# Kernel optimization log

Measured on AMD Instinct MI355X. Metric: run time of the kernel, lower is better.

Reference implementation:

```python
import jax, jax.numpy as jnp
import numpy as np

THRESHOLD = 0.3          # config.sparse_threshold
COMPETITION_FACTOR = 2.0 # config.competition_factor
TARGET_SPARSITY = 0.1    # config.target_sparsity


def setup_inputs() -> dict:
    key = jax.random.key(0)
    B, D = 32768, 1024
    H = D // 4
    ks = jax.random.split(key, 18)
    def lin(k, fan_in, shape):
        return jax.random.normal(k, shape, dtype=jnp.float32) / np.sqrt(fan_in)
    return {
        "features": jax.random.normal(ks[0], (B, D), dtype=jnp.float32),
        # sparse_gating: Linear(D, D//4) -> ReLU -> Linear(D//4, D) -> Sigmoid
        "w_g1": lin(ks[1], D, (D, H)), "b_g1": jnp.zeros((H,), jnp.float32),
        "w_g2": lin(ks[2], H, (H, D)), "b_g2": jnp.zeros((D,), jnp.float32),
        # competition_calculator: Linear(D, D) -> ReLU -> Linear(D, 1) -> Sigmoid
        "w_c1": lin(ks[3], D, (D, D)), "b_c1": jnp.zeros((D,), jnp.float32),
        "w_c2": lin(ks[4], D, (D, 1)), "b_c2": jnp.zeros((1,), jnp.float32),
        # sparsity_feedback: Linear(2, 16) -> ReLU -> Linear(16, D) -> Sigmoid
        "w_r1": lin(ks[5], 2, (2, 16)), "b_r1": jnp.zeros((16,), jnp.float32),
        "w_r2": lin(ks[6], 16, (16, D)), "b_r2": jnp.zeros((D,), jnp.float32),
        # adaptive_threshold: Linear(3, 16) -> ReLU -> Linear(16, 1) -> Sigmoid
        "w_m1": lin(ks[7], 3, (3, 16)), "b_m1": jnp.zeros((16,), jnp.float32),
        "w_m2": lin(ks[8], 16, (16, 1)), "b_m2": jnp.zeros((1,), jnp.float32),
    }


def _competitive_sparse(f, w_c1, b_c1, w_c2, b_c2):
    # competition_strength: [B, 1] scalar per row (output Linear has out_dim 1)
    c = jax.nn.sigmoid(jax.nn.relu(f @ w_c1 + b_c1) @ w_c2 + b_c2)  # [B,1]
    inh = COMPETITION_FACTOR * c                                     # [B,1]
    # other_activations_j = f_j * (1 - inh) for j != i, and f_i at position i.
    scaled = f * (1.0 - inh)                                         # [B,D]
    # max over j != i of scaled_j, vectorized via top-2
    top2_vals, _ = jax.lax.top_k(scaled, 2)                          # [B,2]
    am = jnp.argmax(scaled, axis=-1)                                 # [B]
    idx = jnp.arange(f.shape[-1])
    max_excl = jnp.where(idx[None, :] == am[:, None],
                         top2_vals[:, 1:2], top2_vals[:, 0:1])       # [B,D]
    other_max = jnp.maximum(f, max_excl)                             # includes own f_i term
    win = other_max < f
    return jnp.where(f > THRESHOLD, jnp.where(win, f, 0.0), f)


def reference(features, w_g1, b_g1, w_g2, b_g2, w_c1, b_c1, w_c2, b_c2,
              w_r1, b_r1, w_r2, b_r2, w_m1, b_m1, w_m2, b_m2):
    # 1) sparse gating
    gw = jax.nn.sigmoid(jax.nn.relu(features @ w_g1 + b_g1) @ w_g2 + b_g2)
    gated = features * gw
    # 2) competitive sparse activation
    comp = _competitive_sparse(gated, w_c1, b_c1, w_c2, b_c2)
    # 3) dynamic sparsity regulation
    cur_sp = jnp.mean((jnp.abs(comp) < 0.1).astype(comp.dtype), axis=-1)  # [B]
    sp_in = jnp.stack([cur_sp, jnp.full_like(cur_sp, TARGET_SPARSITY)], axis=-1)  # [B,2]
    rw = jax.nn.sigmoid(jax.nn.relu(sp_in @ w_r1 + b_r1) @ w_r2 + b_r2)  # [B,D]
    dyn = comp * rw
    # 4) adaptive threshold (monitor); torch.std is unbiased -> ddof=1
    fmean = jnp.mean(dyn, axis=-1, keepdims=True)
    fstd = jnp.std(dyn, axis=-1, ddof=1, keepdims=True)
    fmax = jnp.max(dyn, axis=-1, keepdims=True)
    thr_in = jnp.concatenate([fmean, fstd, fmax], axis=-1)            # [B,3]
    thr = jax.nn.sigmoid(jax.nn.relu(thr_in @ w_m1 + b_m1) @ w_m2 + b_m2)  # [B,1]
    # 5) final sparse mask
    mask = (jnp.abs(dyn) > thr).astype(dyn.dtype)
    return dyn * mask
```

## Files before the change

### kernel.cpp

```cpp
#include <hip/hip_runtime.h>
#include <cmath>

#define TM 128
#define TN 128
#define TK 16
#define LDSW 132
#define FIXCAP 262144u
#define ROWCAP 32768u

#define B03  2.5e-5f
#define B01  2.5e-5f
#define B2   5e-6
#define BDYN 3e-5f

#define STAGE_STORE(B)                                                          \
        As[B][aq * 4 + 0][ar] = pa0.x; As[B][aq * 4 + 1][ar] = pa0.y;           \
        As[B][aq * 4 + 2][ar] = pa0.z; As[B][aq * 4 + 3][ar] = pa0.w;           \
        As[B][aq * 4 + 0][ar + 64] = pa1.x; As[B][aq * 4 + 1][ar + 64] = pa1.y; \
        As[B][aq * 4 + 2][ar + 64] = pa1.z; As[B][aq * 4 + 3][ar + 64] = pa1.w; \
        *(float4*)&Bs[B][bk][bn4] = pb0;                                        \
        *(float4*)&Bs[B][bk + 8][bn4] = pb1;

#define GEMM_MAINLOOP(Aptr, Wptr, Kdim, Ndim)                                   \
    __shared__ float As[2][TK][LDSW];                                           \
    __shared__ float Bs[2][TK][LDSW];                                           \
    const int tid = threadIdx.x;                                                \
    const int bm = blockIdx.x * TM;                                             \
    const int bn = blockIdx.y * TN;                                             \
    const int tx = tid & 15, ty = tid >> 4;                                     \
    const int ar = tid >> 2, aq = tid & 3;                                      \
    const int bk = tid >> 5, bn4 = (tid & 31) * 4;                              \
    float acc[2][2][4][4];                                                      \
    _Pragma("unroll") for (int a = 0; a < 2; ++a)                               \
    _Pragma("unroll") for (int b = 0; b < 2; ++b)                               \
    _Pragma("unroll") for (int i = 0; i < 4; ++i)                               \
    _Pragma("unroll") for (int j = 0; j < 4; ++j) acc[a][b][i][j] = 0.f;        \
    float4 pa0 = *(const float4*)((Aptr) + (size_t)(bm + ar) * (Kdim) + aq * 4);      \
    float4 pa1 = *(const float4*)((Aptr) + (size_t)(bm + ar + 64) * (Kdim) + aq * 4); \
    float4 pb0 = *(const float4*)((Wptr) + (size_t)bk * (Ndim) + bn + bn4);           \
    float4 pb1 = *(const float4*)((Wptr) + (size_t)(bk + 8) * (Ndim) + bn + bn4);     \
    STAGE_STORE(0)                                                              \
    __syncthreads();                                                            \
    int buf = 0;                                                                \
    for (int k0 = 0; k0 < (Kdim); k0 += TK) {                                   \
        const int nk = k0 + TK;                                                 \
        if (nk < (Kdim)) {                                                      \
            pa0 = *(const float4*)((Aptr) + (size_t)(bm + ar) * (Kdim) + nk + aq * 4);      \
            pa1 = *(const float4*)((Aptr) + (size_t)(bm + ar + 64) * (Kdim) + nk + aq * 4); \
            pb0 = *(const float4*)((Wptr) + (size_t)(nk + bk) * (Ndim) + bn + bn4);         \
            pb1 = *(const float4*)((Wptr) + (size_t)(nk + bk + 8) * (Ndim) + bn + bn4);     \
        }                                                                       \
        _Pragma("unroll") for (int k = 0; k < TK; ++k) {                        \
            float4 da0 = *(const float4*)&As[buf][k][ty * 4];                   \
            float4 da1 = *(const float4*)&As[buf][k][64 + ty * 4];              \
            float4 db0 = *(const float4*)&Bs[buf][k][tx * 4];                   \
            float4 db1 = *(const float4*)&Bs[buf][k][64 + tx * 4];              \
            const float* dap[2] = {&da0.x, &da1.x};                             \
            const float* dbp[2] = {&db0.x, &db1.x};                             \
            _Pragma("unroll") for (int a = 0; a < 2; ++a)                       \
            _Pragma("unroll") for (int b = 0; b < 2; ++b)                       \
            _Pragma("unroll") for (int i = 0; i < 4; ++i)                       \
            _Pragma("unroll") for (int j = 0; j < 4; ++j)                       \
                acc[a][b][i][j] = fmaf(dap[a][i], dbp[b][j], acc[a][b][i][j]);  \
        }                                                                       \
        if (nk < (Kdim)) {                                                      \
            const int nb = buf ^ 1;                                             \
            STAGE_STORE(nb)                                                     \
            __syncthreads();                                                    \
            buf = nb;                                                           \
        }                                                                       \
    }

__global__ __launch_bounds__(256) void gemm1_f32(
    const float* __restrict__ A, const float* __restrict__ W,
    const float* __restrict__ bias, float* __restrict__ out, int M)
{
    const int K = 1024, N = 256;
    GEMM_MAINLOOP(A, W, K, N)
    #pragma unroll
    for (int a = 0; a < 2; ++a) {
        #pragma unroll
        for (int b = 0; b < 2; ++b) {
            const int col = bn + b * 64 + tx * 4;
            float4 bi = *(const float4*)(bias + col);
            #pragma unroll
            for (int i = 0; i < 4; ++i) {
                const int row = bm + a * 64 + ty * 4 + i;
                float4 o;
                o.x = fmaxf(acc[a][b][i][0] + bi.x, 0.f);
                o.y = fmaxf(acc[a][b][i][1] + bi.y, 0.f);
                o.z = fmaxf(acc[a][b][i][2] + bi.z, 0.f);
                o.w = fmaxf(acc[a][b][i][3] + bi.w, 0.f);
                *(float4*)(out + (size_t)row * N + col) = o;
            }
        }
    }
}

__global__ __launch_bounds__(256) void gemm2_f32(
    const float* __restrict__ A, const float* __restrict__ W,
    const float* __restrict__ bias, const float* __restrict__ F,
    float* __restrict__ out, unsigned* __restrict__ ectr1,
    uint2* __restrict__ elist1, int M)
{
    const int K = 256, N = 1024;
    GEMM_MAINLOOP(A, W, K, N)
    #pragma unroll
    for (int a = 0; a < 2; ++a) {
        #pragma unroll
        for (int b = 0; b < 2; ++b) {
            const int col = bn + b * 64 + tx * 4;
            float4 bi = *(const float4*)(bias + col);
            const float* bip = &bi.x;
            #pragma unroll
            for (int i = 0; i < 4; ++i) {
                const int row = bm + a * 64 + ty * 4 + i;
                float4 fv = *(const float4*)(F + (size_t)row * N + col);
                const float* fvp = &fv.x;
                float4 o;
                float* op = &o.x;
                #pragma unroll
                for (int j = 0; j < 4; ++j) {
                    float z = acc[a][b][i][j] + bip[j];
                    float gw = 1.0f / (1.0f + __expf(-z));
                    float g = fvp[j] * gw;
                    float c = (g > 0.3f) ? 0.f : g;
                    if (fabsf(g - 0.3f) < B03 || fabsf(fabsf(c) - 0.1f) < B01) {
                        unsigned idx = atomicAdd(ectr1, 1u);
                        if (idx < FIXCAP) elist1[idx] = make_uint2((unsigned)row, (unsigned)(col + j));
                    }
                    op[j] = c;
                }
                *(float4*)(out + (size_t)row * N + col) = o;
            }
        }
    }
}

__global__ __launch_bounds__(256) void fix_near(
    const float* __restrict__ h1, const float* __restrict__ F,
    const float* __restrict__ Wg2, const float* __restrict__ bg2,
    const unsigned* __restrict__ ectr1, const uint2* __restrict__ elist1,
    unsigned* __restrict__ ectr2, uint2* __restrict__ elist2,
    float* __restrict__ out, int* __restrict__ corr)
{
    __shared__ double red[4];
    const int tid = threadIdx.x;
    unsigned cnt = *ectr1;
    if (cnt > FIXCAP) cnt = FIXCAP;

    for (unsigned e = blockIdx.x; e < cnt; e += gridDim.x) {
        const unsigned row = elist1[e].x, col = elist1[e].y;
        double p = (double)h1[(size_t)row * 256 + tid]
                 * (double)Wg2[(size_t)tid * 1024 + col];
        #pragma unroll
        for (int o = 32; o > 0; o >>= 1) p += __shfl_down(p, o, 64);
        if ((tid & 63) == 0) red[tid >> 6] = p;
        __syncthreads();
        if (tid == 0) {
            double z2 = red[0] + red[1] + red[2] + red[3] + (double)bg2[col];
            double gw = 1.0 / (1.0 + exp(-z2));
            double g = (double)F[(size_t)row * 1024 + col] * gw;
            double c = (g > 0.3) ? 0.0 : g;
            bool near = (fabs(g - 0.3) < B2) || (fabs(fabs(c) - 0.1) < B2);
            if (near) {
                unsigned i2 = atomicAdd(ectr2, 1u);
                if (i2 < FIXCAP) elist2[i2] = make_uint2(row, col);
            } else {
                float cf = (float)c;
                int d_ref = (fabs(c) < 0.1) ? 1 : 0;
                int d_st  = (fabsf(cf) < 0.1f) ? 1 : 0;
                if (d_ref != d_st) atomicAdd(&corr[row], d_ref - d_st);
                out[(size_t)row * 1024 + col] = cf;
            }
        }
        __syncthreads();
    }
}

#define WT_PREFETCH(ptr)                                                        \
            r0 = *(const float4*)((ptr) + 0 * 1024 + tid * 4);                  \
            r1 = *(const float4*)((ptr) + 1 * 1024 + tid * 4);                  \
            r2 = *(const float4*)((ptr) + 2 * 1024 + tid * 4);                  \
            r3 = *(const float4*)((ptr) + 3 * 1024 + tid * 4);

#define WT_STORE(B)                                                             \
            *(float4*)&Wt[B][0 * 1024 + tid * 4] = r0;                          \
            *(float4*)&Wt[B][1 * 1024 + tid * 4] = r1;                          \
            *(float4*)&Wt[B][2 * 1024 + tid * 4] = r2;                          \
            *(float4*)&Wt[B][3 * 1024 + tid * 4] = r3;

__global__ __launch_bounds__(256) void fix_full(
    const float* __restrict__ F, const float* __restrict__ Wg1,
    const float* __restrict__ bg1, const float* __restrict__ Wg2,
    const float* __restrict__ bg2,
    const unsigned* __restrict__ ectr2, const uint2* __restrict__ elist2,
    float* __restrict__ out, int* __restrict__ corr)
{
    __shared__ float Fs[1024];
    __shared__ float Wt[2][4096];
    __shared__ double red[4];
    const int tid = threadIdx.x;
    unsigned cnt = *ectr2;
    if (cnt > FIXCAP) cnt = FIXCAP;

    for (unsigned e = blockIdx.x; e < cnt; e += gridDim.x) {
        const unsigned row = elist2[e].x, col = elist2[e].y;
        __syncthreads();
        *(float4*)&Fs[tid * 4] = *(const float4*)(F + (size_t)row * 1024 + tid * 4);

        float4 r0, r1, r2, r3;
        WT_PREFETCH(Wg1)
        WT_STORE(0)
        __syncthreads();
        double p0 = 0.0, p1 = 0.0, p2 = 0.0, p3 = 0.0;
        int buf = 0;
        for (int t = 0; t < 64; ++t) {
            if (t + 1 < 64) { const float* np = Wg1 + (size_t)(t + 1) * 4096; WT_PREFETCH(np) }
            const int kb = t * 16;
            #pragma unroll
            for (int kk = 0; kk < 16; kk += 4) {
                p0 += (double)Fs[kb + kk + 0] * (double)Wt[buf][(kk + 0) * 256 + tid];
                p1 += (double)Fs[kb + kk + 1] * (double)Wt[buf][(kk + 1) * 256 + tid];
                p2 += (double)Fs[kb + kk + 2] * (double)Wt[buf][(kk + 2) * 256 + tid];
                p3 += (double)Fs[kb + kk + 3] * (double)Wt[buf][(kk + 3) * 256 + tid];
            }
            if (t + 1 < 64) {
                const int nb = buf ^ 1;
                WT_STORE(nb)
                __syncthreads();
                buf = nb;
            }
        }
        double h = ((p0 + p1) + (p2 + p3)) + (double)bg1[tid];
        h = (h > 0.0) ? h : 0.0;
        double p = h * (double)Wg2[(size_t)tid * 1024 + col];
        #pragma unroll
        for (int o = 32; o > 0; o >>= 1) p += __shfl_down(p, o, 64);
        if ((tid & 63) == 0) red[tid >> 6] = p;
        __syncthreads();
        if (tid == 0) {
            double z2 = red[0] + red[1] + red[2] + red[3] + (double)bg2[col];
            double gw = 1.0 / (1.0 + exp(-z2));
            double g = (double)Fs[col] * gw;
            double c = (g > 0.3) ? 0.0 : g;
            float cf = (float)c;
            int d_ref = (fabs(c) < 0.1) ? 1 : 0;
            int d_st  = (fabsf(cf) < 0.1f) ? 1 : 0;
            if (d_ref != d_st) atomicAdd(&corr[row], d_ref - d_st);
            out[(size_t)row * 1024 + col] = cf;
        }
    }
}

__global__ __launch_bounds__(256) void finalize_rows(
    float* __restrict__ C,
    const float* __restrict__ wr1, const float* __restrict__ br1,
    const float* __restrict__ wr2, const float* __restrict__ br2,
    const float* __restrict__ wm1, const float* __restrict__ bm1,
    const float* __restrict__ wm2, const float* __restrict__ bm2,
    const int* __restrict__ corr,
    unsigned* __restrict__ rctr, unsigned* __restrict__ rowlist)
{
    const int D = 1024;
    const int tid = threadIdx.x;
    const int lane = tid & 63;
    const unsigned row = blockIdx.x * 4 + (tid >> 6);
    const size_t base = (size_t)row * D;
    const int col0 = lane * 4;

    float4 c4[4];
    #pragma unroll
    for (int q = 0; q < 4; ++q)
        c4[q] = *(const float4*)(C + base + q * 256 + col0);

    float c[16];
    #pragma unroll
    for (int q = 0; q < 4; ++q) {
        c[q * 4 + 0] = c4[q].x; c[q * 4 + 1] = c4[q].y;
        c[q * 4 + 2] = c4[q].z; c[q * 4 + 3] = c4[q].w;
    }

    float cnt = 0.f;
    #pragma unroll
    for (int i = 0; i < 16; ++i) cnt += (fabsf(c[i]) < 0.1f) ? 1.f : 0.f;
    #pragma unroll
    for (int o = 32; o > 0; o >>= 1) cnt += __shfl_xor(cnt, o, 64);
    cnt += (float)corr[row];
    const double cur_sp = (double)cnt / 1024.0;

    float hid[16];
    #pragma unroll
    for (int h = 0; h < 16; ++h) {
        double z = cur_sp * (double)wr1[h] + 0.1 * (double)wr1[16 + h] + (double)br1[h];
        hid[h] = (float)((z > 0.0) ? z : 0.0);
    }

    float dyn[16];
    #pragma unroll
    for (int q = 0; q < 4; ++q) {
        const int cq = q * 256 + col0;
        float4 b4 = *(const float4*)(br2 + cq);
        float z[4] = {b4.x, b4.y, b4.z, b4.w};
        #pragma unroll
        for (int h = 0; h < 16; ++h) {
            float4 w4 = *(const float4*)(wr2 + (size_t)h * D + cq);
            z[0] = fmaf(hid[h], w4.x, z[0]);
            z[1] = fmaf(hid[h], w4.y, z[1]);
            z[2] = fmaf(hid[h], w4.z, z[2]);
            z[3] = fmaf(hid[h], w4.w, z[3]);
        }
        #pragma unroll
        for (int j = 0; j < 4; ++j) {
            float rw = 1.0f / (1.0f + __expf(-z[j]));
            dyn[q * 4 + j] = c[q * 4 + j] * rw;
        }
    }

    float s = 0.f, mx = -1e30f;
    #pragma unroll
    for (int i = 0; i < 16; ++i) { s += dyn[i]; mx = fmaxf(mx, dyn[i]); }
    #pragma unroll
    for (int o = 32; o > 0; o >>= 1) s += __shfl_xor(s, o, 64);
    const float mean = s / 1024.0f;

    float sq = 0.f;
    #pragma unroll
    for (int i = 0; i < 16; ++i) { float d = dyn[i] - mean; sq = fmaf(d, d, sq); }
    #pragma unroll
    for (int o = 32; o > 0; o >>= 1) sq += __shfl_xor(sq, o, 64);
    const float sd = sqrtf(sq / 1023.0f);

    #pragma unroll
    for (int o = 32; o > 0; o >>= 1) mx = fmaxf(mx, __shfl_xor(mx, o, 64));

    double acc2 = (double)bm2[0];
    #pragma unroll
    for (int h = 0; h < 16; ++h) {
        double hz = (double)mean * (double)wm1[h] + (double)sd * (double)wm1[16 + h]
                  + (double)mx * (double)wm1[32 + h] + (double)bm1[h];
        hz = (hz > 0.0) ? hz : 0.0;
        acc2 += hz * (double)wm2[h];
    }
    const float thr = (float)(1.0 / (1.0 + exp(-acc2)));

    bool fl = false;
    #pragma unroll
    for (int i = 0; i < 16; ++i)
        if (fabsf(fabsf(dyn[i]) - thr) < BDYN) fl = true;

    if (__any(fl)) {
        if (lane == 0) {
            unsigned idx = atomicAdd(rctr, 1u);
            if (idx < ROWCAP) rowlist[idx] = row;
        }
        return;
    }

    #pragma unroll
    for (int q = 0; q < 4; ++q) {
        float4 o4;
        float* op = &o4.x;
        #pragma unroll
        for (int j = 0; j < 4; ++j) {
            float d = dyn[q * 4 + j];
            op[j] = (fabsf(d) > thr) ? d : 0.f;
        }
        *(float4*)(C + base + q * 256 + col0) = o4;
    }
}

__device__ __forceinline__ double block_reduce_d(double v, double* sm, int tid, int op)
{
    #pragma unroll
    for (int o = 32; o > 0; o >>= 1) {
        double other = __shfl_down(v, o, 64);
        v = op ? fmax(v, other) : (v + other);
    }
    if ((tid & 63) == 0) sm[tid >> 6] = v;
    __syncthreads();
    if (tid == 0) {
        double r = sm[0];
        for (int w = 1; w < 4; ++w) r = op ? fmax(r, sm[w]) : (r + sm[w]);
        sm[4] = r;
    }
    __syncthreads();
    double r = sm[4];
    __syncthreads();
    return r;
}

__global__ __launch_bounds__(256) void row_exact(
    const float* __restrict__ F,
    const float* __restrict__ wg1, const float* __restrict__ bg1,
    const float* __restrict__ wg2, const float* __restrict__ bg2,
    const float* __restrict__ wr1, const float* __restrict__ br1,
    const float* __restrict__ wr2, const float* __restrict__ br2,
    const float* __restrict__ wm1, const float* __restrict__ bm1,
    const float* __restrict__ wm2, const float* __restrict__ bm2,
    const unsigned* __restrict__ rctr, const unsigned* __restrict__ rowlist,
    float* __restrict__ out)
{
    __shared__ float  Fs[1024];
    __shared__ float  Wt[2][4096];
    __shared__ double h1d[256];
    __shared__ double sm[8];
    const int tid = threadIdx.x;
    unsigned rcnt = *rctr;
    if (rcnt > ROWCAP) rcnt = ROWCAP;

    for (unsigned e = blockIdx.x; e < rcnt; e += gridDim.x) {
        const unsigned row = rowlist[e];
        __syncthreads();
        *(float4*)&Fs[tid * 4] = *(const float4*)(F + (size_t)row * 1024 + tid * 4);

        {
            float4 r0, r1, r2, r3;
            WT_PREFETCH(wg1)
            WT_STORE(0)
            __syncthreads();
            double p0 = 0.0, p1 = 0.0, p2 = 0.0, p3 = 0.0;
            int buf = 0;
            for (int t = 0; t < 64; ++t) {
                if (t + 1 < 64) { const float* np = wg1 + (size_t)(t + 1) * 4096; WT_PREFETCH(np) }
                const int kb = t * 16;
                #pragma unroll
                for (int kk = 0; kk < 16; kk += 4) {
                    p0 += (double)Fs[kb + kk + 0] * (double)Wt[buf][(kk + 0) * 256 + tid];
                    p1 += (double)Fs[kb + kk + 1] * (double)Wt[buf][(kk + 1) * 256 + tid];
                    p2 += (double)Fs[kb + kk + 2] * (double)Wt[buf][(kk + 2) * 256 + tid];
                    p3 += (double)Fs[kb + kk + 3] * (double)Wt[buf][(kk + 3) * 256 + tid];
                }
                if (t + 1 < 64) {
                    const int nb = buf ^ 1;
                    WT_STORE(nb)
                    __syncthreads();
                    buf = nb;
                }
            }
            double a = ((p0 + p1) + (p2 + p3)) + (double)bg1[tid];
            h1d[tid] = (a > 0.0) ? a : 0.0;
        }
        __syncthreads();

        const int c0 = tid * 4;
        double zA[4] = {0.0, 0.0, 0.0, 0.0};
        double zB[4] = {0.0, 0.0, 0.0, 0.0};
        {
            float4 r0, r1, r2, r3;
            WT_PREFETCH(wg2)
            WT_STORE(0)
            __syncthreads();
            int buf = 0;
            for (int t = 0; t < 64; ++t) {
                if (t + 1 < 64) { const float* np = wg2 + (size_t)(t + 1) * 4096; WT_PREFETCH(np) }
                const int jb = t * 4;
                #pragma unroll
                for (int kk = 0; kk < 4; kk += 2) {
                    float4 wA = *(const float4*)&Wt[buf][(kk + 0) * 1024 + c0];
                    float4 wB = *(const float4*)&Wt[buf][(kk + 1) * 1024 + c0];
                    double hA = h1d[jb + kk], hB = h1d[jb + kk + 1];
                    zA[0] += hA * (double)wA.x; zA[1] += hA * (double)wA.y;
                    zA[2] += hA * (double)wA.z; zA[3] += hA * (double)wA.w;
                    zB[0] += hB * (double)wB.x; zB[1] += hB * (double)wB.y;
                    zB[2] += hB * (double)wB.z; zB[3] += hB * (double)wB.w;
                }
                if (t + 1 < 64) {
                    const int nb = buf ^ 1;
                    WT_STORE(nb)
                    __syncthreads();
                    buf = nb;
                }
            }
        }
        double comp[4];
        double cnt = 0.0;
        #pragma unroll
        for (int j = 0; j < 4; ++j) {
            double z2v = (double)bg2[c0 + j] + zA[j] + zB[j];
            double gw = 1.0 / (1.0 + exp(-z2v));
            double g = (double)Fs[c0 + j] * gw;
            double cm = (g > 0.3) ? 0.0 : g;
            comp[j] = cm;
            cnt += (fabs(cm) < 0.1) ? 1.0 : 0.0;
        }
        cnt = block_reduce_d(cnt, sm, tid, 0);
        const double cur_sp = cnt / 1024.0;

        double hid[16];
        #pragma unroll
        for (int h = 0; h < 16; ++h) {
            double hz = cur_sp * (double)wr1[h] + 0.1 * (double)wr1[16 + h] + (double)br1[h];
            hid[h] = (hz > 0.0) ? hz : 0.0;
        }
        double zr[4] = {(double)br2[c0], (double)br2[c0 + 1],
                        (double)br2[c0 + 2], (double)br2[c0 + 3]};
        #pragma unroll
        for (int h = 0; h < 16; ++h) {
            float4 w4 = *(const float4*)(wr2 + (size_t)h * 1024 + c0);
            zr[0] += hid[h] * (double)w4.x; zr[1] += hid[h] * (double)w4.y;
            zr[2] += hid[h] * (double)w4.z; zr[3] += hid[h] * (double)w4.w;
        }
        double dyn[4];
        #pragma unroll
        for (int j = 0; j < 4; ++j) {
            double rw = 1.0 / (1.0 + exp(-zr[j]));
            dyn[j] = comp[j] * rw;
        }

        double s = dyn[0] + dyn[1] + dyn[2] + dyn[3];
        s = block_reduce_d(s, sm, tid, 0);
        const double mean = s / 1024.0;

        double sq = 0.0;
        #pragma unroll
        for (int j = 0; j < 4; ++j) { double d = dyn[j] - mean; sq += d * d; }
        sq = block_reduce_d(sq, sm, tid, 0);
        const double sd = sqrt(sq / 1023.0);

        double mx = fmax(fmax(dyn[0], dyn[1]), fmax(dyn[2], dyn[3]));
        mx = block_reduce_d(mx, sm, tid, 1);

        double acc2 = (double)bm2[0];
        #pragma unroll
        for (int h = 0; h < 16; ++h) {
            double hz = mean * (double)wm1[h] + sd * (double)wm1[16 + h]
                      + mx * (double)wm1[32 + h] + (double)bm1[h];
            hz = (hz > 0.0) ? hz : 0.0;
            acc2 += hz * (double)wm2[h];
        }
        const double thr = 1.0 / (1.0 + exp(-acc2));

        float4 o4;
        o4.x = (float)((fabs(dyn[0]) > thr) ? dyn[0] : 0.0);
        o4.y = (float)((fabs(dyn[1]) > thr) ? dyn[1] : 0.0);
        o4.z = (float)((fabs(dyn[2]) > thr) ? dyn[2] : 0.0);
        o4.w = (float)((fabs(dyn[3]) > thr) ? dyn[3] : 0.0);
        *(float4*)(out + (size_t)row * 1024 + c0) = o4;
    }
}

extern "C" void kernel_launch(void* const* d_in, const int* in_sizes, int n_in,
                              void* d_out, int out_size, void* d_ws, size_t ws_size,
                              hipStream_t stream)
{
    const float* F   = (const float*)d_in[0];
    const float* wg1 = (const float*)d_in[1];
    const float* bg1 = (const float*)d_in[2];
    const float* wg2 = (const float*)d_in[3];
    const float* bg2 = (const float*)d_in[4];
    const float* wr1 = (const float*)d_in[9];
    const float* br1 = (const float*)d_in[10];
    const float* wr2 = (const float*)d_in[11];
    const float* br2 = (const float*)d_in[12];
    const float* wm1 = (const float*)d_in[13];
    const float* bm1 = (const float*)d_in[14];
    const float* wm2 = (const float*)d_in[15];
    const float* bm2 = (const float*)d_in[16];

    float* out = (float*)d_out;
    const int M = in_sizes[0] / 1024;

    char* ws = (char*)d_ws;
    float*    h1      = (float*)ws;
    uint2*    elist1  = (uint2*)(ws + (32u << 20));
    uint2*    elist2  = (uint2*)(ws + (34u << 20));
    unsigned* rowlist = (unsigned*)(ws + (36u << 20));
    int*      corr    = (int*)(ws + (36u << 20) + (128u << 10));
    unsigned* ctrs    = (unsigned*)(ws + (36u << 20) + (256u << 10));
    unsigned* ectr1 = ctrs, *ectr2 = ctrs + 1, *rctr = ctrs + 2;

    hipMemsetAsync(corr, 0, (size_t)M * sizeof(int) + 16, stream);
    gemm1_f32<<<dim3(M / TM, 256 / TN), 256, 0, stream>>>(F, wg1, bg1, h1, M);
    gemm2_f32<<<dim3(M / TM, 1024 / TN), 256, 0, stream>>>(h1, wg2, bg2, F, out, ectr1, elist1, M);
    fix_near<<<2048, 256, 0, stream>>>(h1, F, wg2, bg2, ectr1, elist1, ectr2, elist2, out, corr);
    fix_full<<<1024, 256, 0, stream>>>(F, wg1, bg1, wg2, bg2, ectr2, elist2, out, corr);
    finalize_rows<<<M / 4, 256, 0, stream>>>(out, wr1, br1, wr2, br2, wm1, bm1, wm2, bm2,
                                             corr, rctr, rowlist);
    row_exact<<<2048, 256, 0, stream>>>(F, wg1, bg1, wg2, bg2, wr1, br1, wr2, br2,
                                        wm1, bm1, wm2, bm2, rctr, rowlist, out);
}
```

Measured before the change: 960.6 us.

## Run second gating GEMM on bf16x3 MFMA with split-precision operands

Replaces the FP32 SIMT second gating GEMM with a matrix-core kernel that emulates FP32 by splitting each operand into high and low bf16 parts and summing three MFMA products. A new pre-pass splits and transposes the second weight matrix into bf16 hi/lo buffers, and the activation tile is split on the fly while loading into LDS. The existing near-threshold correction path still rechecks borderline entries. The second fix list capacity is halved to fit the new workspace layout, which risks dropping entries if more than that many need the full recompute.

```diff
diff --git a/kernel.cpp b/kernel.cpp
--- a/kernel.cpp
+++ b/kernel.cpp
@@ -5,13 +5,29 @@
 #define TN 128
 #define TK 16
 #define LDSW 132
-#define FIXCAP 262144u
+#define FIXCAP  262144u
+#define FIXCAP2 131072u
 #define ROWCAP 32768u
 
 #define B03  2.5e-5f
 #define B01  2.5e-5f
 #define B2   5e-6
 #define BDYN 3e-5f
+
+typedef __attribute__((ext_vector_type(8))) short bf16x8;
+typedef __attribute__((ext_vector_type(8))) unsigned short ushort8;
+typedef __attribute__((ext_vector_type(4))) float f32x4;
+
+__device__ __forceinline__ unsigned short bf16_rne(float x)
+{
+    unsigned u = __float_as_uint(x);
+    unsigned r = u + 0x7FFFu + ((u >> 16) & 1u);
+    return (unsigned short)(r >> 16);
+}
+__device__ __forceinline__ float bf16_to_f(unsigned short h)
+{
+    return __uint_as_float(((unsigned)h) << 16);
+}
 
 #define STAGE_STORE(B)                                                          \
         As[B][aq * 4 + 0][ar] = pa0.x; As[B][aq * 4 + 1][ar] = pa0.y;           \
@@ -97,41 +113,120 @@
     }
 }
 
-__global__ __launch_bounds__(256) void gemm2_f32(
-    const float* __restrict__ A, const float* __restrict__ W,
-    const float* __restrict__ bias, const float* __restrict__ F,
-    float* __restrict__ out, unsigned* __restrict__ ectr1,
-    uint2* __restrict__ elist1, int M)
-{
-    const int K = 256, N = 1024;
-    GEMM_MAINLOOP(A, W, K, N)
-    #pragma unroll
-    for (int a = 0; a < 2; ++a) {
-        #pragma unroll
-        for (int b = 0; b < 2; ++b) {
-            const int col = bn + b * 64 + tx * 4;
-            float4 bi = *(const float4*)(bias + col);
-            const float* bip = &bi.x;
+__global__ __launch_bounds__(256) void split_wg2(
+    const float* __restrict__ wg2, unsigned short* __restrict__ th,
+    unsigned short* __restrict__ tl)
+{
+    const int n = blockIdx.x;
+    const int k = threadIdx.x;
+    float x = wg2[(size_t)k * 1024 + n];
+    unsigned short h = bf16_rne(x);
+    th[(size_t)n * 256 + k] = h;
+    tl[(size_t)n * 256 + k] = bf16_rne(x - bf16_to_f(h));
+}
+
+__global__ __launch_bounds__(256) void gemm2_mfma(
+    const float* __restrict__ h1, const unsigned short* __restrict__ bTh,
+    const unsigned short* __restrict__ bTl, const float* __restrict__ bias,
+    const float* __restrict__ F, float* __restrict__ out,
+    unsigned* __restrict__ ectr1, uint2* __restrict__ elist1, int M)
+{
+    __shared__ __align__(16) unsigned short Ah[128][40];
+    __shared__ __align__(16) unsigned short Al[128][40];
+    __shared__ __align__(16) unsigned short Bh[128][40];
+    __shared__ __align__(16) unsigned short Bl[128][40];
+
+    const int tid  = threadIdx.x;
+    const int lane = tid & 63;
+    const int wave = tid >> 6;
+    const int wr = wave >> 1, wc = wave & 1;
+    const int bm = blockIdx.x * 128;
+    const int bn = blockIdx.y * 128;
+
+    f32x4 acc[4][4];
+    #pragma unroll
+    for (int mi = 0; mi < 4; ++mi)
+        #pragma unroll
+        for (int ni = 0; ni < 4; ++ni)
+            acc[mi][ni] = (f32x4){0.f, 0.f, 0.f, 0.f};
+
+    const int sr = tid >> 1;
+    const int sh = tid & 1;
+
+    for (int k0 = 0; k0 < 256; k0 += 32) {
+        __syncthreads();
+        {
+            const float* src = h1 + (size_t)(bm + sr) * 256 + k0 + sh * 16;
+            unsigned short* dh = &Ah[sr][sh * 16];
+            unsigned short* dl = &Al[sr][sh * 16];
             #pragma unroll
-            for (int i = 0; i < 4; ++i) {
-                const int row = bm + a * 64 + ty * 4 + i;
-                float4 fv = *(const float4*)(F + (size_t)row * N + col);
-                const float* fvp = &fv.x;
-                float4 o;
-                float* op = &o.x;
+            for (int i = 0; i < 2; ++i) {
+                float4 f0 = ((const float4*)src)[2 * i + 0];
+                float4 f1 = ((const float4*)src)[2 * i + 1];
+                float xs[8] = {f0.x, f0.y, f0.z, f0.w, f1.x, f1.y, f1.z, f1.w};
+                ushort8 vh, vl;
                 #pragma unroll
-                for (int j = 0; j < 4; ++j) {
-                    float z = acc[a][b][i][j] + bip[j];
-                    float gw = 1.0f / (1.0f + __expf(-z));
-                    float g = fvp[j] * gw;
-                    float c = (g > 0.3f) ? 0.f : g;
-                    if (fabsf(g - 0.3f) < B03 || fabsf(fabsf(c) - 0.1f) < B01) {
-                        unsigned idx = atomicAdd(ectr1, 1u);
-                        if (idx < FIXCAP) elist1[idx] = make_uint2((unsigned)row, (unsigned)(col + j));
-                    }
-                    op[j] = c;
+                for (int j = 0; j < 8; ++j) {
+                    unsigned short hh = bf16_rne(xs[j]);
+                    vh[j] = hh;
+                    vl[j] = bf16_rne(xs[j] - bf16_to_f(hh));
                 }
-                *(float4*)(out + (size_t)row * N + col) = o;
+                ((ushort8*)dh)[i] = vh;
+                ((ushort8*)dl)[i] = vl;
+            }
+        }
+        {
+            const ushort8* s0 = (const ushort8*)(bTh + (size_t)(bn + sr) * 256 + k0 + sh * 16);
+            const ushort8* s1 = (const ushort8*)(bTl + (size_t)(bn + sr) * 256 + k0 + sh * 16);
+            ushort8* d0 = (ushort8*)&Bh[sr][sh * 16];
+            ushort8* d1 = (ushort8*)&Bl[sr][sh * 16];
+            d0[0] = s0[0]; d0[1] = s0[1];
+            d1[0] = s1[0]; d1[1] = s1[1];
+        }
+        __syncthreads();
+
+        const int ko = (lane >> 4) * 8;
+        const int fr = lane & 15;
+        bf16x8 ah[4], al[4], bh[4], bl[4];
+        #pragma unroll
+        for (int mi = 0; mi < 4; ++mi) {
+            ah[mi] = *(const bf16x8*)&Ah[wr * 64 + mi * 16 + fr][ko];
+            al[mi] = *(const bf16x8*)&Al[wr * 64 + mi * 16 + fr][ko];
+        }
+        #pragma unroll
+        for (int ni = 0; ni < 4; ++ni) {
+            bh[ni] = *(const bf16x8*)&Bh[wc * 64 + ni * 16 + fr][ko];
+            bl[ni] = *(const bf16x8*)&Bl[wc * 64 + ni * 16 + fr][ko];
+        }
+        #pragma unroll
+        for (int mi = 0; mi < 4; ++mi) {
+            #pragma unroll
+            for (int ni = 0; ni < 4; ++ni) {
+                acc[mi][ni] = __builtin_amdgcn_mfma_f32_16x16x32_bf16(ah[mi], bh[ni], acc[mi][ni], 0, 0, 0);
+                acc[mi][ni] = __builtin_amdgcn_mfma_f32_16x16x32_bf16(ah[mi], bl[ni], acc[mi][ni], 0, 0, 0);
+                acc[mi][ni] = __builtin_amdgcn_mfma_f32_16x16x32_bf16(al[mi], bh[ni], acc[mi][ni], 0, 0, 0);
+            }
+        }
+    }
+
+    #pragma unroll
+    for (int ni = 0; ni < 4; ++ni) {
+        const int col = bn + wc * 64 + ni * 16 + (lane & 15);
+        const float bi = bias[col];
+        #pragma unroll
+        for (int mi = 0; mi < 4; ++mi) {
+            #pragma unroll
+            for (int r = 0; r < 4; ++r) {
+                const int row = bm + wr * 64 + mi * 16 + (lane >> 4) * 4 + r;
+                float z = acc[mi][ni][r] + bi;
+                float gw = 1.0f / (1.0f + __expf(-z));
+                float g = F[(size_t)row * 1024 + col] * gw;
+                float c = (g > 0.3f) ? 0.f : g;
+                if (fabsf(g - 0.3f) < B03 || fabsf(fabsf(c) - 0.1f) < B01) {
+                    unsigned idx = atomicAdd(ectr1, 1u);
+                    if (idx < FIXCAP) elist1[idx] = make_uint2((unsigned)row, (unsigned)col);
+                }
+                out[(size_t)row * 1024 + col] = c;
             }
         }
     }
@@ -165,7 +260,7 @@
             bool near = (fabs(g - 0.3) < B2) || (fabs(fabs(c) - 0.1) < B2);
             if (near) {
                 unsigned i2 = atomicAdd(ectr2, 1u);
-                if (i2 < FIXCAP) elist2[i2] = make_uint2(row, col);
+                if (i2 < FIXCAP2) elist2[i2] = make_uint2(row, col);
             } else {
                 float cf = (float)c;
                 int d_ref = (fabs(c) < 0.1) ? 1 : 0;
@@ -202,7 +297,7 @@
     __shared__ double red[4];
     const int tid = threadIdx.x;
     unsigned cnt = *ectr2;
-    if (cnt > FIXCAP) cnt = FIXCAP;
+    if (cnt > FIXCAP2) cnt = FIXCAP2;
 
     for (unsigned e = blockIdx.x; e < cnt; e += gridDim.x) {
         const unsigned row = elist2[e].x, col = elist2[e].y;
@@ -562,17 +657,21 @@
     const int M = in_sizes[0] / 1024;
 
     char* ws = (char*)d_ws;
-    float*    h1      = (float*)ws;
-    uint2*    elist1  = (uint2*)(ws + (32u << 20));
-    uint2*    elist2  = (uint2*)(ws + (34u << 20));
-    unsigned* rowlist = (unsigned*)(ws + (36u << 20));
-    int*      corr    = (int*)(ws + (36u << 20) + (128u << 10));
-    unsigned* ctrs    = (unsigned*)(ws + (36u << 20) + (256u << 10));
+    float*          h1      = (float*)ws;
+    uint2*          elist1  = (uint2*)(ws + (32u << 20));
+    unsigned short* wg2Th   = (unsigned short*)(ws + (34u << 20));
+    unsigned short* wg2Tl   = (unsigned short*)(ws + (34u << 20) + (512u << 10));
+    uint2*          elist2  = (uint2*)(ws + (35u << 20));
+    unsigned*       rowlist = (unsigned*)(ws + (36u << 20));
+    int*            corr    = (int*)(ws + (36u << 20) + (128u << 10));
+    unsigned*       ctrs    = (unsigned*)(ws + (36u << 20) + (256u << 10));
     unsigned* ectr1 = ctrs, *ectr2 = ctrs + 1, *rctr = ctrs + 2;
 
     hipMemsetAsync(corr, 0, (size_t)M * sizeof(int) + 16, stream);
+    split_wg2<<<1024, 256, 0, stream>>>(wg2, wg2Th, wg2Tl);
     gemm1_f32<<<dim3(M / TM, 256 / TN), 256, 0, stream>>>(F, wg1, bg1, h1, M);
-    gemm2_f32<<<dim3(M / TM, 1024 / TN), 256, 0, stream>>>(h1, wg2, bg2, F, out, ectr1, elist1, M);
+    gemm2_mfma<<<dim3(M / 128, 1024 / 128), 256, 0, stream>>>(h1, wg2Th, wg2Tl, bg2, F,
+                                                              out, ectr1, elist1, M);
     fix_near<<<2048, 256, 0, stream>>>(h1, F, wg2, bg2, ectr1, elist1, ectr2, elist2, out, corr);
     fix_full<<<1024, 256, 0, stream>>>(F, wg1, bg1, wg2, bg2, ectr2, elist2, out, corr);
     finalize_rows<<<M / 4, 256, 0, stream>>>(out, wr1, br1, wr2, br2, wm1, bm1, wm2, bm2,
```

Result: faster. 909.0 us (-5.4%).
